# Kernel tuning notes

Hardware: AMD Instinct MI355X
Metric: run time of the kernel (lower is better)

Reference implementation:

```python
import jax, jax.numpy as jnp
import numpy as np

N_NODES = 100000
N_EDGES = 1600000
IN_FT = 128
OUT_FT = 32


def setup_inputs() -> dict:
    key = jax.random.key(0)
    k_seq, k_w, k_row, k_col, k_val = jax.random.split(key, 5)
    seq = jax.random.normal(k_seq, (N_NODES, IN_FT), dtype=jnp.float32)
    # xavier_uniform with gain=1.414 for weight [in_ft, out_ft]
    limit = 1.414 * np.sqrt(6.0 / (IN_FT + OUT_FT))
    weight = jax.random.uniform(k_w, (IN_FT, OUT_FT), dtype=jnp.float32,
                                minval=-limit, maxval=limit)
    edge_row = jax.random.randint(k_row, (N_EDGES,), 0, N_NODES, dtype=jnp.int64)
    edge_col = jax.random.randint(k_col, (N_EDGES,), 0, N_NODES, dtype=jnp.int64)
    edge_val = jax.random.uniform(k_val, (N_EDGES,), dtype=jnp.float32)
    return {"seq": seq, "weight": weight, "edge_row": edge_row,
            "edge_col": edge_col, "edge_val": edge_val}


def reference(seq, weight, edge_row, edge_col, edge_val):
    # support = seq @ weight : dense projection [N, out_ft]
    support = seq @ weight
    # out = spmm(adj, support): adj in COO (row, col, val), out[i] = sum_e val_e * support[col_e]
    msgs = edge_val[:, None] * support[edge_col]          # [E, out_ft]
    out = jax.ops.segment_sum(msgs, edge_row, num_segments=N_NODES)
    return jax.nn.relu(out)
```

## Files before the change

kernel.cpp:

```cpp
#include <hip/hip_runtime.h>
#include <hip/hip_bf16.h>
#include <hip/hip_fp16.h>

#define IN_FT  128
#define OUT_FT 32
#define APITCH 136

#define RPB   256
#define CAP   8192
#define BA_T  1024
#define BA_E  4096

typedef _Float16 f16x8 __attribute__((ext_vector_type(8)));
typedef __attribute__((ext_vector_type(4))) float f32x4;

union H2 { unsigned u; _Float16 h[2]; };

__global__ __launch_bounds__(256) void gcn_swz(const float* __restrict__ w,
                                               _Float16* __restrict__ wtab) {
    int t = threadIdx.x;
    for (int i = t; i < 2 * 4 * 64 * 8; i += 256) {
        int j    = i & 7;
        int lane = (i >> 3) & 63;
        int kt   = (i >> 9) & 3;
        int tile = i >> 11;
        int k    = kt * 32 + (lane >> 4) * 8 + j;
        int c    = (lane & 15) + tile * 16;
        wtab[i] = (_Float16)w[k * OUT_FT + c];
    }
}

__global__ __launch_bounds__(256) void gcn_gemm_mfma(const float* __restrict__ seq,
                                                     const _Float16* __restrict__ wtab,
                                                     unsigned short* __restrict__ sup,
                                                     int n) {
    __shared__ __align__(16) _Float16 at[64 * APITCH];
    const int t    = threadIdx.x;
    const int base = blockIdx.x * 64;

    for (int it = 0; it < 4; ++it) {
        int i     = it * 256 + t;
        int row_l = i >> 4;
        int c     = i & 15;
        int row   = base + row_l;
        f16x8 v = (f16x8)0;
        if (row < n) {
            const float4* p = (const float4*)(seq + (size_t)row * IN_FT + c * 8);
            float4 lo = p[0], hi = p[1];
            v[0] = (_Float16)lo.x; v[1] = (_Float16)lo.y;
            v[2] = (_Float16)lo.z; v[3] = (_Float16)lo.w;
            v[4] = (_Float16)hi.x; v[5] = (_Float16)hi.y;
            v[6] = (_Float16)hi.z; v[7] = (_Float16)hi.w;
        }
        *(f16x8*)&at[row_l * APITCH + c * 8] = v;
    }
    __syncthreads();

    const int wave = t >> 6;
    const int lane = t & 63;
    const int m    = lane & 15;
    const int quad = lane >> 4;

    const f16x8* wt = (const f16x8*)wtab;
    const int arow_l = wave * 16 + m;

    f32x4 acc0 = {0.f, 0.f, 0.f, 0.f};
    f32x4 acc1 = {0.f, 0.f, 0.f, 0.f};

    for (int kt = 0; kt < 4; ++kt) {
        f16x8 a  = *(const f16x8*)&at[arow_l * APITCH + kt * 32 + quad * 8];
        f16x8 b0 = wt[(0 * 4 + kt) * 64 + lane];
        f16x8 b1 = wt[(1 * 4 + kt) * 64 + lane];
        acc0 = __builtin_amdgcn_mfma_f32_16x16x32_f16(a, b0, acc0, 0, 0, 0);
        acc1 = __builtin_amdgcn_mfma_f32_16x16x32_f16(a, b1, acc1, 0, 0, 0);
    }

    for (int i = 0; i < 4; ++i) {
        int ro = base + wave * 16 + quad * 4 + i;
        if (ro < n) {
            _Float16 h0 = (_Float16)acc0[i];
            _Float16 h1 = (_Float16)acc1[i];
            sup[(size_t)ro * OUT_FT + m]      = *(unsigned short*)&h0;
            sup[(size_t)ro * OUT_FT + 16 + m] = *(unsigned short*)&h1;
        }
    }
}

__global__ __launch_bounds__(BA_T) void gcn_binA(const int* __restrict__ erow,
                                                 const int* __restrict__ ecol,
                                                 const float* __restrict__ eval,
                                                 int* __restrict__ bptr,
                                                 uint2* __restrict__ ebin, int nE) {
    __shared__ int cnt[512];
    __shared__ int cur[512];
    const int t  = threadIdx.x;
    const int cb = blockIdx.x * BA_E;
    if (t < 512) cnt[t] = 0;
    __syncthreads();

    int r[4];
    unsigned cq[4];
    int nv = 0;
    const int i0 = cb + t * 4;
    if (i0 + 4 <= nE) {
        int4   r4 = *(const int4*)&erow[i0];
        int4   c4 = *(const int4*)&ecol[i0];
        float4 v4 = *(const float4*)&eval[i0];
        r[0] = r4.x; r[1] = r4.y; r[2] = r4.z; r[3] = r4.w;
        cq[0] = ((unsigned)c4.x << 15) | (unsigned)(v4.x * 32767.f + 0.5f);
        cq[1] = ((unsigned)c4.y << 15) | (unsigned)(v4.y * 32767.f + 0.5f);
        cq[2] = ((unsigned)c4.z << 15) | (unsigned)(v4.z * 32767.f + 0.5f);
        cq[3] = ((unsigned)c4.w << 15) | (unsigned)(v4.w * 32767.f + 0.5f);
        nv = 4;
    } else {
        #pragma unroll 4
        for (int k = 0; k < 4; ++k) {
            int i = i0 + k;
            if (i < nE) {
                r[nv]  = erow[i];
                cq[nv] = ((unsigned)ecol[i] << 15)
                       | (unsigned)(eval[i] * 32767.f + 0.5f);
                ++nv;
            }
        }
    }

    #pragma unroll 4
    for (int k = 0; k < 4; ++k)
        if (k < nv) atomicAdd(&cnt[r[k] >> 8], 1);
    __syncthreads();

    if (t < 512 && cnt[t]) cur[t] = atomicAdd(&bptr[t], cnt[t]);
    __syncthreads();

    #pragma unroll 4
    for (int k = 0; k < 4; ++k)
        if (k < nv) {
            int b = r[k] >> 8;
            int p = atomicAdd(&cur[b], 1);
            if (p < CAP) {
                uint2 e;
                e.x = cq[k];
                e.y = (unsigned)(r[k] & 255);
                ebin[(size_t)b * CAP + p] = e;
            }
        }
}

__global__ __launch_bounds__(BA_T) void gcn_acc(const uint2* __restrict__ ebin,
                                                const int* __restrict__ bptr,
                                                const unsigned* __restrict__ sup32,
                                                float2* __restrict__ out, int n) {
    __shared__ unsigned csr[CAP];
    __shared__ int hist[RPB];
    __shared__ int segs[RPB];
    __shared__ int cursor[RPB];
    const int    t    = threadIdx.x;
    const int    b    = blockIdx.x;
    const int    cnt  = min(bptr[b], CAP);
    const size_t base = (size_t)b * CAP;

    if (t < RPB) hist[t] = 0;
    __syncthreads();

    for (int i = t; i < cnt; i += BA_T)
        atomicAdd(&hist[ebin[base + i].y], 1);
    __syncthreads();

    int v = 0;
    if (t < RPB) { v = hist[t]; segs[t] = v; }
    __syncthreads();
    for (int o = 1; o < RPB; o <<= 1) {
        int x = 0;
        if (t < RPB && t >= o) x = segs[t - o];
        __syncthreads();
        if (t < RPB) segs[t] += x;
        __syncthreads();
    }
    if (t < RPB) cursor[t] = segs[t] - v;
    __syncthreads();

    for (int i = t; i < cnt; i += BA_T) {
        uint2 e = ebin[base + i];
        int   p = atomicAdd(&cursor[e.y], 1);
        csr[p] = e.x;
    }
    __syncthreads();

    const int g = t >> 4;
    const int j = t & 15;
    const int rbase = b * RPB;
    for (int rr = g; rr < RPB; rr += BA_T / 16) {
        int end = segs[rr];
        int st  = end - hist[rr];
        float a0 = 0.f, a1 = 0.f;
        int e = st;
        for (; e + 2 <= end; e += 2) {
            unsigned c0 = csr[e], c1 = csr[e + 1];
            H2 s0; s0.u = sup32[(c0 >> 15) * 16 + j];
            H2 s1; s1.u = sup32[(c1 >> 15) * 16 + j];
            float v0 = (float)(c0 & 0x7fffu) * (1.f / 32767.f);
            float v1 = (float)(c1 & 0x7fffu) * (1.f / 32767.f);
            a0 += v0 * (float)s0.h[0] + v1 * (float)s1.h[0];
            a1 += v0 * (float)s0.h[1] + v1 * (float)s1.h[1];
        }
        if (e < end) {
            unsigned c0 = csr[e];
            H2 s0; s0.u = sup32[(c0 >> 15) * 16 + j];
            float v0 = (float)(c0 & 0x7fffu) * (1.f / 32767.f);
            a0 += v0 * (float)s0.h[0];
            a1 += v0 * (float)s0.h[1];
        }
        int row = rbase + rr;
        if (row < n) {
            float2 o;
            o.x = fmaxf(a0, 0.f);
            o.y = fmaxf(a1, 0.f);
            out[(size_t)row * 16 + j] = o;
        }
    }
}

extern "C" void kernel_launch(void* const* d_in, const int* in_sizes, int n_in,
                              void* d_out, int out_size, void* d_ws, size_t ws_size,
                              hipStream_t stream) {
    const float* seq  = (const float*)d_in[0];
    const float* w    = (const float*)d_in[1];
    const int*   erow = (const int*)d_in[2];
    const int*   ecol = (const int*)d_in[3];
    const float* eval = (const float*)d_in[4];
    float* out = (float*)d_out;

    const int n_nodes = in_sizes[0] / IN_FT;
    const int n_edges = in_sizes[2];
    const int nB      = (n_nodes + RPB - 1) / RPB;

    unsigned short* sup  = (unsigned short*)d_ws;
    uint2*          ebin = (uint2*)(sup + (size_t)n_nodes * OUT_FT);
    int*            bptr = (int*)(ebin + (size_t)nB * CAP);
    _Float16*       wtab = (_Float16*)(bptr + 512);

    hipMemsetAsync(bptr, 0, 512 * sizeof(int), stream);

    gcn_swz<<<1, 256, 0, stream>>>(w, wtab);

    gcn_gemm_mfma<<<(n_nodes + 63) / 64, 256, 0, stream>>>(seq, wtab, sup, n_nodes);

    gcn_binA<<<(n_edges + BA_E - 1) / BA_E, BA_T, 0, stream>>>(erow, ecol, eval,
                                                               bptr, ebin, n_edges);

    gcn_acc<<<nB, BA_T, 0, stream>>>(ebin, bptr, (const unsigned*)sup,
                                     (float2*)out, n_nodes);
}
```

Before: 155.6 us.

## Fuse GEMM and edge binning into one heterogeneous launch

```diff
diff --git a/kernel.cpp b/kernel.cpp
--- a/kernel.cpp
+++ b/kernel.cpp
@@ -8,8 +8,8 @@
 
 #define RPB   256
 #define CAP   8192
-#define BA_T  1024
-#define BA_E  4096
+#define ACC_T 1024
+#define BIN_E 4096
 
 typedef _Float16 f16x8 __attribute__((ext_vector_type(8)));
 typedef __attribute__((ext_vector_type(4))) float f32x4;
@@ -30,12 +30,91 @@
     }
 }
 
-__global__ __launch_bounds__(256) void gcn_gemm_mfma(const float* __restrict__ seq,
-                                                     const _Float16* __restrict__ wtab,
-                                                     unsigned short* __restrict__ sup,
-                                                     int n) {
+__global__ __launch_bounds__(256) void gcn_gemm_bin(const float* __restrict__ seq,
+                                                    const _Float16* __restrict__ wtab,
+                                                    unsigned short* __restrict__ sup,
+                                                    const int* __restrict__ erow,
+                                                    const int* __restrict__ ecol,
+                                                    const float* __restrict__ eval,
+                                                    int* __restrict__ bptr,
+                                                    uint2* __restrict__ ebin,
+                                                    int n, int nE, int gb) {
     __shared__ __align__(16) _Float16 at[64 * APITCH];
-    const int t    = threadIdx.x;
+    const int t = threadIdx.x;
+
+    if ((int)blockIdx.x >= gb) {
+        int* cnt = (int*)at;
+        int* cur = cnt + 512;
+        cnt[t] = 0;
+        cnt[t + 256] = 0;
+        __syncthreads();
+
+        const int cb = ((int)blockIdx.x - gb) * BIN_E;
+        const int ce = min(cb + BIN_E, nE);
+
+        #pragma unroll
+        for (int k = 0; k < 4; ++k) {
+            int i0 = cb + (k * 256 + t) * 4;
+            if (i0 + 4 <= ce) {
+                int4 r4 = *(const int4*)&erow[i0];
+                atomicAdd(&cnt[r4.x >> 8], 1);
+                atomicAdd(&cnt[r4.y >> 8], 1);
+                atomicAdd(&cnt[r4.z >> 8], 1);
+                atomicAdd(&cnt[r4.w >> 8], 1);
+            } else {
+                for (int i = i0; i < ce; ++i)
+                    atomicAdd(&cnt[erow[i] >> 8], 1);
+            }
+        }
+        __syncthreads();
+
+        if (cnt[t])       cur[t]       = atomicAdd(&bptr[t],       cnt[t]);
+        if (cnt[t + 256]) cur[t + 256] = atomicAdd(&bptr[t + 256], cnt[t + 256]);
+        __syncthreads();
+
+        #pragma unroll
+        for (int k = 0; k < 4; ++k) {
+            int i0 = cb + (k * 256 + t) * 4;
+            if (i0 + 4 <= ce) {
+                int4   r4 = *(const int4*)&erow[i0];
+                int4   c4 = *(const int4*)&ecol[i0];
+                float4 v4 = *(const float4*)&eval[i0];
+                int      rr[4] = {r4.x, r4.y, r4.z, r4.w};
+                unsigned cq[4];
+                cq[0] = ((unsigned)c4.x << 15) | (unsigned)(v4.x * 32767.f + 0.5f);
+                cq[1] = ((unsigned)c4.y << 15) | (unsigned)(v4.y * 32767.f + 0.5f);
+                cq[2] = ((unsigned)c4.z << 15) | (unsigned)(v4.z * 32767.f + 0.5f);
+                cq[3] = ((unsigned)c4.w << 15) | (unsigned)(v4.w * 32767.f + 0.5f);
+                #pragma unroll
+                for (int q = 0; q < 4; ++q) {
+                    int b = rr[q] >> 8;
+                    int p = atomicAdd(&cur[b], 1);
+                    if (p < CAP) {
+                        uint2 e;
+                        e.x = cq[q];
+                        e.y = (unsigned)(rr[q] & 255);
+                        ebin[(size_t)b * CAP + p] = e;
+                    }
+                }
+            } else {
+                for (int i = i0; i < ce; ++i) {
+                    int      r = erow[i];
+                    unsigned q = ((unsigned)ecol[i] << 15)
+                               | (unsigned)(eval[i] * 32767.f + 0.5f);
+                    int b = r >> 8;
+                    int p = atomicAdd(&cur[b], 1);
+                    if (p < CAP) {
+                        uint2 e;
+                        e.x = q;
+                        e.y = (unsigned)(r & 255);
+                        ebin[(size_t)b * CAP + p] = e;
+                    }
+                }
+            }
+        }
+        return;
+    }
+
     const int base = blockIdx.x * 64;
 
     for (int it = 0; it < 4; ++it) {
@@ -86,71 +165,10 @@
     }
 }
 
-__global__ __launch_bounds__(BA_T) void gcn_binA(const int* __restrict__ erow,
-                                                 const int* __restrict__ ecol,
-                                                 const float* __restrict__ eval,
-                                                 int* __restrict__ bptr,
-                                                 uint2* __restrict__ ebin, int nE) {
-    __shared__ int cnt[512];
-    __shared__ int cur[512];
-    const int t  = threadIdx.x;
-    const int cb = blockIdx.x * BA_E;
-    if (t < 512) cnt[t] = 0;
-    __syncthreads();
-
-    int r[4];
-    unsigned cq[4];
-    int nv = 0;
-    const int i0 = cb + t * 4;
-    if (i0 + 4 <= nE) {
-        int4   r4 = *(const int4*)&erow[i0];
-        int4   c4 = *(const int4*)&ecol[i0];
-        float4 v4 = *(const float4*)&eval[i0];
-        r[0] = r4.x; r[1] = r4.y; r[2] = r4.z; r[3] = r4.w;
-        cq[0] = ((unsigned)c4.x << 15) | (unsigned)(v4.x * 32767.f + 0.5f);
-        cq[1] = ((unsigned)c4.y << 15) | (unsigned)(v4.y * 32767.f + 0.5f);
-        cq[2] = ((unsigned)c4.z << 15) | (unsigned)(v4.z * 32767.f + 0.5f);
-        cq[3] = ((unsigned)c4.w << 15) | (unsigned)(v4.w * 32767.f + 0.5f);
-        nv = 4;
-    } else {
-        #pragma unroll 4
-        for (int k = 0; k < 4; ++k) {
-            int i = i0 + k;
-            if (i < nE) {
-                r[nv]  = erow[i];
-                cq[nv] = ((unsigned)ecol[i] << 15)
-                       | (unsigned)(eval[i] * 32767.f + 0.5f);
-                ++nv;
-            }
-        }
-    }
-
-    #pragma unroll 4
-    for (int k = 0; k < 4; ++k)
-        if (k < nv) atomicAdd(&cnt[r[k] >> 8], 1);
-    __syncthreads();
-
-    if (t < 512 && cnt[t]) cur[t] = atomicAdd(&bptr[t], cnt[t]);
-    __syncthreads();
-
-    #pragma unroll 4
-    for (int k = 0; k < 4; ++k)
-        if (k < nv) {
-            int b = r[k] >> 8;
-            int p = atomicAdd(&cur[b], 1);
-            if (p < CAP) {
-                uint2 e;
-                e.x = cq[k];
-                e.y = (unsigned)(r[k] & 255);
-                ebin[(size_t)b * CAP + p] = e;
-            }
-        }
-}
-
-__global__ __launch_bounds__(BA_T) void gcn_acc(const uint2* __restrict__ ebin,
-                                                const int* __restrict__ bptr,
-                                                const unsigned* __restrict__ sup32,
-                                                float2* __restrict__ out, int n) {
+__global__ __launch_bounds__(ACC_T) void gcn_acc(const uint2* __restrict__ ebin,
+                                                 const int* __restrict__ bptr,
+                                                 const unsigned* __restrict__ sup32,
+                                                 float2* __restrict__ out, int n) {
     __shared__ unsigned csr[CAP];
     __shared__ int hist[RPB];
     __shared__ int segs[RPB];
@@ -163,7 +181,7 @@
     if (t < RPB) hist[t] = 0;
     __syncthreads();
 
-    for (int i = t; i < cnt; i += BA_T)
+    for (int i = t; i < cnt; i += ACC_T)
         atomicAdd(&hist[ebin[base + i].y], 1);
     __syncthreads();
 
@@ -180,7 +198,7 @@
     if (t < RPB) cursor[t] = segs[t] - v;
     __syncthreads();
 
-    for (int i = t; i < cnt; i += BA_T) {
+    for (int i = t; i < cnt; i += ACC_T) {
         uint2 e = ebin[base + i];
         int   p = atomicAdd(&cursor[e.y], 1);
         csr[p] = e.x;
@@ -190,7 +208,7 @@
     const int g = t >> 4;
     const int j = t & 15;
     const int rbase = b * RPB;
-    for (int rr = g; rr < RPB; rr += BA_T / 16) {
+    for (int rr = g; rr < RPB; rr += ACC_T / 16) {
         int end = segs[rr];
         int st  = end - hist[rr];
         float a0 = 0.f, a1 = 0.f;
@@ -244,11 +262,11 @@
 
     gcn_swz<<<1, 256, 0, stream>>>(w, wtab);
 
-    gcn_gemm_mfma<<<(n_nodes + 63) / 64, 256, 0, stream>>>(seq, wtab, sup, n_nodes);
-
-    gcn_binA<<<(n_edges + BA_E - 1) / BA_E, BA_T, 0, stream>>>(erow, ecol, eval,
-                                                               bptr, ebin, n_edges);
-
-    gcn_acc<<<nB, BA_T, 0, stream>>>(ebin, bptr, (const unsigned*)sup,
-                                     (float2*)out, n_nodes);
-}
+    int gb = (n_nodes + 63) / 64;
+    int bb = (n_edges + BIN_E - 1) / BIN_E;
+    gcn_gemm_bin<<<gb + bb, 256, 0, stream>>>(seq, wtab, sup, erow, ecol, eval,
+                                              bptr, ebin, n_nodes, n_edges, gb);
+
+    gcn_acc<<<nB, ACC_T, 0, stream>>>(ebin, bptr, (const unsigned*)sup,
+                                      (float2*)out, n_nodes);
+}
```

Result: slower. 162.5 us (+4.4%).
